# Performance work log

Measured on AMD Instinct MI355X. Metric: run time of the kernel, lower is better.

Reference implementation:

```python
import jax, jax.numpy as jnp
import numpy as np

HEAD_NUM = 16
KEY_DIM = 64
EMBED = 1024
KV_OUT = HEAD_NUM * KEY_DIM  # 1024


def setup_inputs() -> dict:
    key = jax.random.key(0)
    ks = jax.random.split(key, 11)
    B, L, E = 2, 2048, EMBED
    scale = 0.02
    return {
        "query": jax.random.normal(ks[0], (B, L, E), jnp.float32),
        "key": jax.random.normal(ks[1], (B, L, E), jnp.float32),
        "value": jax.random.normal(ks[2], (B, L, E), jnp.float32),
        "W_Query": jax.random.normal(ks[3], (E, KV_OUT), jnp.float32) * scale,
        "W_Key": jax.random.normal(ks[4], (E, KV_OUT), jnp.float32) * scale,
        "W_Value": jax.random.normal(ks[5], (E, KV_OUT), jnp.float32) * scale,
        "W_Output": jax.random.normal(ks[6], (KV_OUT, E), jnp.float32) * scale,
        "B_Query": jnp.zeros((KV_OUT,), jnp.float32),
        "B_Key": jnp.zeros((KV_OUT,), jnp.float32),
        "B_Value": jnp.zeros((KV_OUT,), jnp.float32),
        "B_Output": jnp.zeros((E,), jnp.float32),
    }


def reference(query, key, value, W_Query, W_Key, W_Value, W_Output,
              B_Query, B_Key, B_Value, B_Output):
    B, Lq, E = query.shape
    Lk = key.shape[1]
    H, D = HEAD_NUM, KEY_DIM
    # QKV projections + bias
    q = query @ W_Query + B_Query            # [B, Lq, H*D]
    k = key @ W_Key + B_Key                  # [B, Lk, H*D]
    v = value @ W_Value + B_Value            # [B, Lk, H*D]
    # tf.split(axis=2) per head == reshape to [B, L, H, D]
    q = q.reshape(B, Lq, H, D)
    k = k.reshape(B, Lk, H, D)
    v = v.reshape(B, Lk, H, D)
    # scaled dot-product attention (no mask, dropout=0)
    scores = jnp.einsum("bqhd,bkhd->bhqk", q, k) / (D ** 0.5)
    probs = jax.nn.softmax(scores, axis=-1)
    out = jnp.einsum("bhqk,bkhd->bqhd", probs, v)  # [B, Lq, H, D]
    out = out.reshape(B, Lq, H * D)
    return out @ W_Output + B_Output
```

## Files before the change

kernel.cpp:

```cpp
#include <hip/hip_runtime.h>

using u16 = unsigned short;
using u32 = unsigned int;

typedef __attribute__((ext_vector_type(8))) short bf16x8;
typedef __attribute__((ext_vector_type(4))) float f32x4;
typedef __attribute__((ext_vector_type(4))) u32 u32x4;
typedef __attribute__((ext_vector_type(2))) u32 u32x2;
typedef __attribute__((ext_vector_type(4))) _Float16 f16x4;
typedef __attribute__((ext_vector_type(8))) _Float16 f16x8;

#define MFMA_BF16_K32(a, b, c) __builtin_amdgcn_mfma_f32_16x16x32_bf16((a), (b), (c), 0, 0, 0)
#define MFMA_F16_K32(a, b, c) __builtin_amdgcn_mfma_f32_16x16x32_f16((a), (b), (c), 0, 0, 0)

#define QSCALE 0.18033688011112042f

extern "C" __device__ float __ocml_native_exp2_f32(float);

__device__ __forceinline__ u16 f2bf(float f) {
  u32 u = __builtin_bit_cast(u32, f);
  return (u16)((u + 0x7fffu + ((u >> 16) & 1u)) >> 16);
}

__device__ __forceinline__ u32 pk_f16(float a, float b) {
  auto v = __builtin_amdgcn_cvt_pkrtz(a, b);
  return __builtin_bit_cast(u32, v);
}

__device__ __forceinline__ void load_lds16(const void* g, void* l) {
  __builtin_amdgcn_global_load_lds((__attribute__((address_space(1))) void*)g,
                                   (__attribute__((address_space(3))) void*)l,
                                   16, 0, 0);
}

#define W0 asm volatile("s_waitcnt vmcnt(0)" ::: "memory")
#define W3 asm volatile("s_waitcnt vmcnt(3)" ::: "memory")
#define W4 asm volatile("s_waitcnt vmcnt(4)" ::: "memory")
#define W8 asm volatile("s_waitcnt vmcnt(8)" ::: "memory")
#define LGKM0 asm volatile("s_waitcnt lgkmcnt(0)" ::: "memory")
#define BARRIER                      \
  do {                               \
    __builtin_amdgcn_s_barrier();    \
    asm volatile("" ::: "memory");   \
  } while (0)

__global__ __launch_bounds__(256) void cvt_all_kernel(
    const float* __restrict__ q, const float* __restrict__ k, const float* __restrict__ v,
    u16* __restrict__ oq, u16* __restrict__ ok, u16* __restrict__ ov,
    const float* __restrict__ w0, const float* __restrict__ w1,
    const float* __restrict__ w2, const float* __restrict__ w3,
    u16* __restrict__ d0, u16* __restrict__ d1,
    u16* __restrict__ d2, u16* __restrict__ d3) {
  const int id = blockIdx.x;
  const int tid = threadIdx.x;
  if (id < 6144) {
    const int z = id >> 11, bx = id & 2047;
    const float* s = z == 0 ? q : z == 1 ? k : v;
    u16* d = z == 0 ? oq : z == 1 ? ok : ov;
    int i = (bx * 256 + tid) * 8;
    f32x4 a = *(const f32x4*)(s + i);
    f32x4 b = *(const f32x4*)(s + i + 4);
    u32x4 o;
    o.x = (u32)f2bf(a.x) | ((u32)f2bf(a.y) << 16);
    o.y = (u32)f2bf(a.z) | ((u32)f2bf(a.w) << 16);
    o.z = (u32)f2bf(b.x) | ((u32)f2bf(b.y) << 16);
    o.w = (u32)f2bf(b.z) | ((u32)f2bf(b.w) << 16);
    *(u32x4*)(d + i) = o;
    return;
  }
  __shared__ float t[64][65];
  const int r0 = id - 6144;
  const int z = r0 >> 8, rr0 = r0 & 255;
  const int bx = rr0 & 15, by = rr0 >> 4;
  const float* src = z == 0 ? w0 : z == 1 ? w1 : z == 2 ? w2 : w3;
  u16* dst = z == 0 ? d0 : z == 1 ? d1 : z == 2 ? d2 : d3;
  const float scale = (z == 0) ? QSCALE : 1.0f;
  const int r = tid >> 4, c4 = (tid & 15) * 4;
#pragma unroll
  for (int i = 0; i < 4; ++i) {
    int row = r + i * 16;
    f32x4 vv = *(const f32x4*)(src + (by * 64 + row) * 1024 + bx * 64 + c4);
    t[row][c4 + 0] = vv.x;
    t[row][c4 + 1] = vv.y;
    t[row][c4 + 2] = vv.z;
    t[row][c4 + 3] = vv.w;
  }
  __syncthreads();
  const int rw = tid >> 2, cc = (tid & 3) * 16;
  alignas(16) u16 tmp[16];
#pragma unroll
  for (int j = 0; j < 16; ++j) tmp[j] = f2bf(t[cc + j][rw] * scale);
  u32x4* outp = (u32x4*)(dst + (bx * 64 + rw) * 1024 + by * 64 + cc);
  outp[0] = *(const u32x4*)&tmp[0];
  outp[1] = *(const u32x4*)&tmp[8];
}

#define QKV_STAGE(BUF, KB)                                                    \
  {                                                                           \
    _Pragma("unroll") for (int t = 0; t < 2; ++t) {                           \
      int c = (wave * 2 + t) * 64 + lane;                                     \
      int row = c >> 2, pc = c & 3, sc = pc ^ ((row >> 1) & 3);               \
      load_lds16(A + (m0 + row) * 1024 + (KB) * 32 + sc * 8,                  \
                 &As[BUF][((wave * 2 + t) * 64) * 8]);                        \
    }                                                                         \
    _Pragma("unroll") for (int t = 0; t < 2; ++t) {                           \
      int c = (wave * 2 + t) * 64 + lane;                                     \
      int row = c >> 2, pc = c & 3, sc = pc ^ ((row >> 1) & 3);               \
      load_lds16(Bt + (n0 + row) * 1024 + (KB) * 32 + sc * 8,                 \
                 &Bs[BUF][((wave * 2 + t) * 64) * 8]);                        \
    }                                                                         \
  }

__global__ __launch_bounds__(256) void gemm_qkv_kernel(
    const u16* __restrict__ x0, const u16* __restrict__ x1, const u16* __restrict__ x2,
    const u16* __restrict__ w0, const u16* __restrict__ w1, const u16* __restrict__ w2,
    const float* __restrict__ b0, const float* __restrict__ b1, const float* __restrict__ b2,
    u16* __restrict__ c0, u16* __restrict__ c1, u16* __restrict__ vt) {
  __shared__ u16 As[2][128 * 32];
  __shared__ u16 Bs[2][128 * 32];
  const int lid = blockIdx.x;
  const int xcd = lid & 7, rr = lid >> 3;
  const int nb = rr & 7, slot = rr >> 3;
  const int g = slot * 8 + xcd;
  const int z = g >> 5, m_idx = g & 31;
  const u16* A = z == 0 ? x0 : z == 1 ? x1 : x2;
  const u16* Bt = z == 0 ? w0 : z == 1 ? w1 : w2;
  const float* bias = z == 0 ? b0 : z == 1 ? b1 : b2;
  const float bscale = z == 0 ? QSCALE : 1.0f;
  const int tid = threadIdx.x;
  const int wave = tid >> 6, lane = tid & 63;
  const int l16 = lane & 15, quad = lane >> 4;
  const int wm = wave >> 1, wn = wave & 1;
  const int m0 = m_idx * 128, n0 = nb * 128;

  f32x4 acc[4][4];
  const f32x4 zf = {0.f, 0.f, 0.f, 0.f};
#pragma unroll
  for (int i = 0; i < 4; ++i)
#pragma unroll
    for (int j = 0; j < 4; ++j) acc[i][j] = zf;

  QKV_STAGE(0, 0);
  QKV_STAGE(1, 1);

  const int chq = (l16 >> 1) & 3;
  for (int kb = 0; kb < 32; ++kb) {
    const int cur = kb & 1;
    if (kb < 31) W4; else W0;
    BARRIER;
    bf16x8 af[4], bfv[4];
#pragma unroll
    for (int mt = 0; mt < 4; ++mt)
      af[mt] = *(const bf16x8*)&As[cur][(wm * 64 + mt * 16 + l16) * 32 + (quad ^ chq) * 8];
#pragma unroll
    for (int nt = 0; nt < 4; ++nt)
      bfv[nt] = *(const bf16x8*)&Bs[cur][(wn * 64 + nt * 16 + l16) * 32 + (quad ^ chq) * 8];
#pragma unroll
    for (int mt = 0; mt < 4; ++mt)
#pragma unroll
      for (int nt = 0; nt < 4; ++nt) acc[mt][nt] = MFMA_BF16_K32(af[mt], bfv[nt], acc[mt][nt]);
    LGKM0;
    BARRIER;
    if (kb + 2 < 32) QKV_STAGE(cur, kb + 2);
  }

  float bv[4];
#pragma unroll
  for (int nt = 0; nt < 4; ++nt) bv[nt] = bias[n0 + wn * 64 + nt * 16 + l16] * bscale;
  if (z != 2) {
    u16* C = z == 0 ? c0 : c1;
#pragma unroll
    for (int mt = 0; mt < 4; ++mt)
#pragma unroll
      for (int nt = 0; nt < 4; ++nt)
#pragma unroll
        for (int r = 0; r < 4; ++r) {
          int row = m0 + wm * 64 + mt * 16 + quad * 4 + r;
          int col = n0 + wn * 64 + nt * 16 + l16;
          C[row * 1024 + col] = f2bf(acc[mt][nt][r] + bv[nt]);
        }
  } else {
#pragma unroll
    for (int p = 0; p < 2; ++p) {
#pragma unroll
      for (int nt = 0; nt < 4; ++nt) {
        const int mte = p * 2, mto = p * 2 + 1;
        f16x4 he, ho;
#pragma unroll
        for (int r = 0; r < 4; ++r) {
          he[r] = (_Float16)(acc[mte][nt][r] + bv[nt]);
          ho[r] = (_Float16)(acc[mto][nt][r] + bv[nt]);
        }
        u32x2 hou = __builtin_bit_cast(u32x2, ho);
        u32x2 hox;
        hox.x = (u32)__shfl_xor((int)hou.x, 32);
        hox.y = (u32)__shfl_xor((int)hou.y, 32);
        int kvb = m0 + wm * 64 + mte * 16 + quad * 4;
        int bb = kvb >> 11, kv = kvb & 2047;
        int kb2 = kv >> 7, w = (kv >> 5) & 3;
        int col = n0 + wn * 64 + nt * 16 + l16;
        int h = col >> 6, dt = (col >> 4) & 3, ld = col & 15;
        int pair = bb * 16 + h;
        u32x2 heu = __builtin_bit_cast(u32x2, he);
        u32x4 outv;
        outv.x = heu.x;
        outv.y = heu.y;
        outv.z = hox.x;
        outv.w = hox.y;
        u16* dst = vt + ((((pair * 16 + kb2) * 4 + w) * 4 + dt) * 512) + (quad * 16 + ld) * 8;
        *(u32x4*)dst = outv;
      }
    }
  }
}

#define OUT_STAGE(BUF, KB)                                                    \
  {                                                                           \
    {                                                                         \
      int c = wave * 64 + lane;                                               \
      int row = c >> 2, pc = c & 3, sc = pc ^ ((row >> 1) & 3);               \
      load_lds16(A + (m0 + row) * 1024 + (KB) * 32 + sc * 8,                  \
                 &As[BUF][(wave * 64) * 8]);                                  \
    }                                                                         \
    _Pragma("unroll") for (int t = 0; t < 2; ++t) {                           \
      int c = (wave * 2 + t) * 64 + lane;                                     \
      int row = c >> 2, pc = c & 3, sc = pc ^ ((row >> 1) & 3);               \
      load_lds16(Bt + (n0 + row) * 1024 + (KB) * 32 + sc * 8,                 \
                 &Bs[BUF][((wave * 2 + t) * 64) * 8]);                        \
    }                                                                         \
  }

__global__ __launch_bounds__(256) void gemm_out_kernel(const u16* __restrict__ A,
                                                       const u16* __restrict__ Bt,
                                                       const float* __restrict__ bias,
                                                       float* __restrict__ C) {
  __shared__ u16 As[2][64 * 32];
  __shared__ u16 Bs[2][128 * 32];
  const int lid = blockIdx.x;
  const int xcd = lid & 7, rr = lid >> 3;
  const int nb = rr & 7, slot = rr >> 3;
  const int by = slot * 8 + xcd;
  const int tid = threadIdx.x;
  const int wave = tid >> 6, lane = tid & 63;
  const int l16 = lane & 15, quad = lane >> 4;
  const int m0 = by * 64, n0 = nb * 128;

  f32x4 acc[4][2];
  const f32x4 zf = {0.f, 0.f, 0.f, 0.f};
#pragma unroll
  for (int i = 0; i < 4; ++i)
#pragma unroll
    for (int j = 0; j < 2; ++j) acc[i][j] = zf;

  OUT_STAGE(0, 0);
  OUT_STAGE(1, 1);

  const int chq = (l16 >> 1) & 3;
  for (int kb = 0; kb < 32; ++kb) {
    const int cur = kb & 1;
    if (kb < 31) W3; else W0;
    BARRIER;
    bf16x8 af[4], bfv[2];
#pragma unroll
    for (int mt = 0; mt < 4; ++mt)
      af[mt] = *(const bf16x8*)&As[cur][(mt * 16 + l16) * 32 + (quad ^ chq) * 8];
#pragma unroll
    for (int nt = 0; nt < 2; ++nt)
      bfv[nt] = *(const bf16x8*)&Bs[cur][(wave * 32 + nt * 16 + l16) * 32 + (quad ^ chq) * 8];
#pragma unroll
    for (int mt = 0; mt < 4; ++mt)
#pragma unroll
      for (int nt = 0; nt < 2; ++nt) acc[mt][nt] = MFMA_BF16_K32(af[mt], bfv[nt], acc[mt][nt]);
    LGKM0;
    BARRIER;
    if (kb + 2 < 32) OUT_STAGE(cur, kb + 2);
  }

  float bv[2];
#pragma unroll
  for (int nt = 0; nt < 2; ++nt) bv[nt] = bias[n0 + wave * 32 + nt * 16 + l16];
#pragma unroll
  for (int mt = 0; mt < 4; ++mt)
#pragma unroll
    for (int nt = 0; nt < 2; ++nt)
#pragma unroll
      for (int r = 0; r < 4; ++r) {
        int row = m0 + mt * 16 + quad * 4 + r;
        int col = n0 + wave * 32 + nt * 16 + l16;
        C[row * 1024 + col] = acc[mt][nt][r] + bv[nt];
      }
}

#define QK_EXP(CUR)                                                               \
  _Pragma("unroll") for (int c2 = 0; c2 < 2; ++c2) {                              \
    const int chunk = wave * 2 + c2;                                              \
    f32x4 s_acc[4];                                                               \
    _Pragma("unroll") for (int qn = 0; qn < 4; ++qn) s_acc[qn] = zf;              \
    _Pragma("unroll") for (int ks = 0; ks < 2; ++ks) {                            \
      bf16x8 kf = *(const bf16x8*)&k_lds[CUR][(chunk * 16 + l16) * 64 +           \
                                              ((ks * 4 + quad) ^ l7) * 8];        \
      _Pragma("unroll") for (int qn = 0; qn < 4; ++qn)                            \
        s_acc[qn] = MFMA_BF16_K32(kf, qf[qn][ks], s_acc[qn]);                     \
    }                                                                             \
    _Pragma("unroll") for (int qn = 0; qn < 4; ++qn) {                            \
      float e0 = __ocml_native_exp2_f32(s_acc[qn].x);                             \
      float e1 = __ocml_native_exp2_f32(s_acc[qn].y);                             \
      float e2 = __ocml_native_exp2_f32(s_acc[qn].z);                             \
      float e3 = __ocml_native_exp2_f32(s_acc[qn].w);                             \
      lp[qn] += (e0 + e1) + (e2 + e3);                                            \
      if (c2 == 0) {                                                              \
        p01[qn] = pk_f16(e0, e1);                                                 \
        p23[qn] = pk_f16(e2, e3);                                                 \
      } else {                                                                    \
        s01[qn] = pk_f16(e0, e1);                                                 \
        s23[qn] = pk_f16(e2, e3);                                                 \
      }                                                                           \
    }                                                                             \
  }

#define FLASH_BODY(KB, CUR, VCUR, VNXT, PFV, PFK, WAIT)                           \
  {                                                                               \
    BARRIER;                                                                      \
    if (PFV) {                                                                    \
      const u16* vp = Vh + ((KB) + 1) * 8192;                                     \
      _Pragma("unroll") for (int dt = 0; dt < 4; ++dt)                            \
        VNXT[dt] = *(const f16x8*)(vp + (wave * 4 + dt) * 512 + lane * 8);        \
    }                                                                             \
    u32 p01[4], p23[4], s01[4], s23[4];                                           \
    QK_EXP(CUR)                                                                   \
    f16x8 paf[4];                                                                 \
    _Pragma("unroll") for (int qn = 0; qn < 4; ++qn) {                            \
      u32x4 tv;                                                                   \
      tv.x = p01[qn];                                                             \
      tv.y = p23[qn];                                                             \
      tv.z = (u32)__shfl_xor((int)s01[qn], 32);                                   \
      tv.w = (u32)__shfl_xor((int)s23[qn], 32);                                   \
      paf[qn] = __builtin_bit_cast(f16x8, tv);                                    \
    }                                                                             \
    LGKM0;                                                                        \
    BARRIER;                                                                      \
    if (PFK) {                                                                    \
      const int kv0 = ((KB) + 2) * 128;                                           \
      _Pragma("unroll") for (int t = 0; t < 4; ++t) {                             \
        int c = (t * 4 + wave) * 64 + lane;                                       \
        int row = c >> 3, sc8 = (c & 7) ^ (row & 7);                              \
        load_lds16(Kh + (kv0 + row) * 1024 + sc8 * 8,                             \
                   &k_lds[CUR][((t * 4 + wave) * 64) * 8]);                       \
      }                                                                           \
    }                                                                             \
    WAIT;                                                                         \
    _Pragma("unroll") for (int dt = 0; dt < 4; ++dt)                              \
      _Pragma("unroll") for (int qn = 0; qn < 4; ++qn)                            \
        o_acc[qn][dt] = MFMA_F16_K32(paf[qn], VCUR[dt], o_acc[qn][dt]);           \
  }

__global__ __launch_bounds__(256, 2) void flash_kernel(const u16* __restrict__ Q,
                                                       const u16* __restrict__ K,
                                                       const u16* __restrict__ Vt,
                                                       u16* __restrict__ O) {
  __shared__ u16 k_lds[2][128 * 64];
  __shared__ float lred[4][64];
  __shared__ float lfin[64];
  const int tid = threadIdx.x;
  const int wave = tid >> 6, lane = tid & 63;
  const int l16 = lane & 15, quad = lane >> 4;
  const int l7 = l16 & 7;
  const int id = blockIdx.x;
  const int xcd = id & 7, slot = id >> 3;
  const int pair = xcd * 4 + (slot & 3);
  const int qb = slot >> 2;
  const int b = pair >> 4, h = pair & 15;
  const u16* Qh = Q + (b * 2048 + qb * 64) * 1024 + h * 64;
  const u16* Kh = K + b * 2048 * 1024 + h * 64;
  const u16* Vh = Vt + pair * 131072;

#pragma unroll
  for (int t = 0; t < 2; ++t) {
    int c = (t * 4 + wave) * 64 + lane;
    int row = c >> 3, sc8 = (c & 7) ^ (row & 7);
    load_lds16(Qh + row * 1024 + sc8 * 8, &k_lds[0][((t * 4 + wave) * 64) * 8]);
  }
  W0;
  __syncthreads();
  bf16x8 qf[4][2];
#pragma unroll
  for (int qn = 0; qn < 4; ++qn)
#pragma unroll
    for (int ks = 0; ks < 2; ++ks)
      qf[qn][ks] = *(const bf16x8*)&k_lds[0][(qn * 16 + l16) * 64 + (((ks * 4 + quad) ^ l7)) * 8];
  __syncthreads();

#pragma unroll
  for (int t = 0; t < 4; ++t) {
    int c = (t * 4 + wave) * 64 + lane;
    int row = c >> 3, sc8 = (c & 7) ^ (row & 7);
    load_lds16(Kh + row * 1024 + sc8 * 8, &k_lds[0][((t * 4 + wave) * 64) * 8]);
  }
  f16x8 vregA[4], vregB[4];
#pragma unroll
  for (int dt = 0; dt < 4; ++dt)
    vregA[dt] = *(const f16x8*)(Vh + (wave * 4 + dt) * 512 + lane * 8);
#pragma unroll
  for (int t = 0; t < 4; ++t) {
    int c = (t * 4 + wave) * 64 + lane;
    int row = c >> 3, sc8 = (c & 7) ^ (row & 7);
    load_lds16(Kh + (128 + row) * 1024 + sc8 * 8, &k_lds[1][((t * 4 + wave) * 64) * 8]);
  }
  W8;

  f32x4 o_acc[4][4];
  const f32x4 zf = {0.f, 0.f, 0.f, 0.f};
#pragma unroll
  for (int qn = 0; qn < 4; ++qn)
#pragma unroll
    for (int dt = 0; dt < 4; ++dt) o_acc[qn][dt] = zf;
  float lp[4] = {0.f, 0.f, 0.f, 0.f};

  for (int kb2 = 0; kb2 < 7; ++kb2) {
    const int kb = kb2 * 2;
    FLASH_BODY(kb, 0, vregA, vregB, true, true, W8);
    FLASH_BODY(kb + 1, 1, vregB, vregA, true, true, W8);
  }
  FLASH_BODY(14, 0, vregA, vregB, true, false, W4);
  FLASH_BODY(15, 1, vregB, vregA, false, false, W0);

#pragma unroll
  for (int qn = 0; qn < 4; ++qn) {
    lp[qn] += __shfl_xor(lp[qn], 16);
    lp[qn] += __shfl_xor(lp[qn], 32);
  }
  if (quad == 0) {
#pragma unroll
    for (int qn = 0; qn < 4; ++qn) lred[wave][qn * 16 + l16] = lp[qn];
  }
  float* bufA = (float*)&k_lds[0][0];
  float* bufB = (float*)&k_lds[1][0];
  if (wave == 1 || wave == 3) {
    float* buf = (wave == 1) ? bufA : bufB;
#pragma unroll
    for (int qm = 0; qm < 4; ++qm)
#pragma unroll
      for (int dt = 0; dt < 4; ++dt)
        *(f32x4*)&buf[(((qm * 4 + dt) * 4 + quad) * 16 + l16) * 4] = o_acc[qm][dt];
  }
  __syncthreads();
  if (tid < 64) lfin[tid] = lred[0][tid] + lred[1][tid] + lred[2][tid] + lred[3][tid];
  if (wave == 0 || wave == 2) {
    float* buf = (wave == 0) ? bufA : bufB;
#pragma unroll
    for (int qm = 0; qm < 4; ++qm)
#pragma unroll
      for (int dt = 0; dt < 4; ++dt)
        o_acc[qm][dt] += *(const f32x4*)&buf[(((qm * 4 + dt) * 4 + quad) * 16 + l16) * 4];
  }
  __syncthreads();
  if (wave == 2) {
#pragma unroll
    for (int qm = 0; qm < 4; ++qm)
#pragma unroll
      for (int dt = 0; dt < 4; ++dt)
        *(f32x4*)&bufA[(((qm * 4 + dt) * 4 + quad) * 16 + l16) * 4] = o_acc[qm][dt];
  }
  __syncthreads();
  if (wave == 0) {
#pragma unroll
    for (int qm = 0; qm < 4; ++qm)
#pragma unroll
      for (int dt = 0; dt < 4; ++dt)
        o_acc[qm][dt] += *(const f32x4*)&bufA[(((qm * 4 + dt) * 4 + quad) * 16 + l16) * 4];
#pragma unroll
    for (int qm = 0; qm < 4; ++qm)
#pragma unroll
      for (int r = 0; r < 4; ++r) {
        int qrow = qm * 16 + quad * 4 + r;
        float inv = 1.0f / lfin[qrow];
        int row = b * 2048 + qb * 64 + qrow;
#pragma unroll
        for (int dt = 0; dt < 4; ++dt)
          O[row * 1024 + h * 64 + dt * 16 + l16] = f2bf(o_acc[qm][dt][r] * inv);
      }
  }
}

extern "C" void kernel_launch(void* const* d_in, const int* in_sizes, int n_in,
                              void* d_out, int out_size, void* d_ws, size_t ws_size,
                              hipStream_t stream) {
  const float* q = (const float*)d_in[0];
  const float* k = (const float*)d_in[1];
  const float* v = (const float*)d_in[2];
  const float* Wq = (const float*)d_in[3];
  const float* Wk = (const float*)d_in[4];
  const float* Wv = (const float*)d_in[5];
  const float* Wo = (const float*)d_in[6];
  const float* Bq = (const float*)d_in[7];
  const float* Bk = (const float*)d_in[8];
  const float* Bv = (const float*)d_in[9];
  const float* Bo = (const float*)d_in[10];
  float* out = (float*)d_out;

  char* w = (char*)d_ws;
  const size_t MB = 1u << 20;
  u16* xq = (u16*)(w + 0 * MB);
  u16* xk = (u16*)(w + 8 * MB);
  u16* xv = (u16*)(w + 16 * MB);
  u16* wqt = (u16*)(w + 24 * MB);
  u16* wkt = (u16*)(w + 26 * MB);
  u16* wvt = (u16*)(w + 28 * MB);
  u16* wot = (u16*)(w + 30 * MB);
  u16* Qp = (u16*)(w + 32 * MB);
  u16* Kp = (u16*)(w + 40 * MB);
  u16* Vtr = (u16*)(w + 48 * MB);
  u16* At = (u16*)(w + 56 * MB);

  cvt_all_kernel<<<dim3(7168), 256, 0, stream>>>(q, k, v, xq, xk, xv,
                                                 Wq, Wk, Wv, Wo, wqt, wkt, wvt, wot);
  gemm_qkv_kernel<<<dim3(768), 256, 0, stream>>>(xq, xk, xv, wqt, wkt, wvt,
                                                 Bq, Bk, Bv, Qp, Kp, Vtr);
  flash_kernel<<<dim3(1024), 256, 0, stream>>>(Qp, Kp, Vtr, At);
  gemm_out_kernel<<<dim3(512), 256, 0, stream>>>(At, wot, Bo, out);
}
```

Measured before the change: 218.4 us.

## Fuse fp32-to-bf16 activation conversion into QKV GEMM A-tile loading

Removes the separate conversion pass over the query, key and value activations. The QKV GEMM now loads fp32 A tiles into registers, converts them to bf16 and writes them to LDS itself, using a register double-buffered pipeline with hand-tuned vmcnt waits. This drops a full read and write of the three activation tensors, which is 72 MB of traffic. In exchange each GEMM block re-reads fp32 A once per N-block, which doubles A bytes per tile. It also adds register pressure and VALU conversion work inside the main loop.

```diff
diff --git a/kernel.cpp b/kernel.cpp
--- a/kernel.cpp
+++ b/kernel.cpp
@@ -34,8 +34,10 @@
 }
 
 #define W0 asm volatile("s_waitcnt vmcnt(0)" ::: "memory")
+#define W2 asm volatile("s_waitcnt vmcnt(2)" ::: "memory")
 #define W3 asm volatile("s_waitcnt vmcnt(3)" ::: "memory")
 #define W4 asm volatile("s_waitcnt vmcnt(4)" ::: "memory")
+#define W6 asm volatile("s_waitcnt vmcnt(6)" ::: "memory")
 #define W8 asm volatile("s_waitcnt vmcnt(8)" ::: "memory")
 #define LGKM0 asm volatile("s_waitcnt lgkmcnt(0)" ::: "memory")
 #define BARRIER                      \
@@ -44,32 +46,14 @@
     asm volatile("" ::: "memory");   \
   } while (0)
 
-__global__ __launch_bounds__(256) void cvt_all_kernel(
-    const float* __restrict__ q, const float* __restrict__ k, const float* __restrict__ v,
-    u16* __restrict__ oq, u16* __restrict__ ok, u16* __restrict__ ov,
+__global__ __launch_bounds__(256) void cvt_w_kernel(
     const float* __restrict__ w0, const float* __restrict__ w1,
     const float* __restrict__ w2, const float* __restrict__ w3,
     u16* __restrict__ d0, u16* __restrict__ d1,
     u16* __restrict__ d2, u16* __restrict__ d3) {
-  const int id = blockIdx.x;
   const int tid = threadIdx.x;
-  if (id < 6144) {
-    const int z = id >> 11, bx = id & 2047;
-    const float* s = z == 0 ? q : z == 1 ? k : v;
-    u16* d = z == 0 ? oq : z == 1 ? ok : ov;
-    int i = (bx * 256 + tid) * 8;
-    f32x4 a = *(const f32x4*)(s + i);
-    f32x4 b = *(const f32x4*)(s + i + 4);
-    u32x4 o;
-    o.x = (u32)f2bf(a.x) | ((u32)f2bf(a.y) << 16);
-    o.y = (u32)f2bf(a.z) | ((u32)f2bf(a.w) << 16);
-    o.z = (u32)f2bf(b.x) | ((u32)f2bf(b.y) << 16);
-    o.w = (u32)f2bf(b.z) | ((u32)f2bf(b.w) << 16);
-    *(u32x4*)(d + i) = o;
-    return;
-  }
   __shared__ float t[64][65];
-  const int r0 = id - 6144;
+  const int r0 = blockIdx.x;
   const int z = r0 >> 8, rr0 = r0 & 255;
   const int bx = rr0 & 15, by = rr0 >> 4;
   const float* src = z == 0 ? w0 : z == 1 ? w1 : z == 2 ? w2 : w3;
@@ -95,24 +79,65 @@
   outp[1] = *(const u32x4*)&tmp[8];
 }
 
-#define QKV_STAGE(BUF, KB)                                                    \
+#define QKV_ISSUE_A(AREG, KB)                                                 \
+  _Pragma("unroll") for (int t = 0; t < 2; ++t) {                             \
+    int c = (wave * 2 + t) * 64 + lane;                                       \
+    int row = c >> 2, pc = c & 3, sc = pc ^ ((row >> 1) & 3);                 \
+    const float* asrc = Af + (m0 + row) * 1024 + (KB) * 32 + sc * 8;          \
+    AREG[t][0] = *(const f32x4*)asrc;                                         \
+    AREG[t][1] = *(const f32x4*)(asrc + 4);                                   \
+  }
+
+#define QKV_ISSUE_B(BUF, KB)                                                  \
+  _Pragma("unroll") for (int t = 0; t < 2; ++t) {                             \
+    int c = (wave * 2 + t) * 64 + lane;                                       \
+    int row = c >> 2, pc = c & 3, sc = pc ^ ((row >> 1) & 3);                 \
+    load_lds16(Bt + (n0 + row) * 1024 + (KB) * 32 + sc * 8,                   \
+               &Bs[BUF][((wave * 2 + t) * 64) * 8]);                          \
+  }
+
+#define QKV_COMMIT_A(AREG, BUF)                                               \
+  _Pragma("unroll") for (int t = 0; t < 2; ++t) {                             \
+    int c = (wave * 2 + t) * 64 + lane;                                       \
+    u32x4 o;                                                                  \
+    o.x = (u32)f2bf(AREG[t][0].x) | ((u32)f2bf(AREG[t][0].y) << 16);          \
+    o.y = (u32)f2bf(AREG[t][0].z) | ((u32)f2bf(AREG[t][0].w) << 16);          \
+    o.z = (u32)f2bf(AREG[t][1].x) | ((u32)f2bf(AREG[t][1].y) << 16);          \
+    o.w = (u32)f2bf(AREG[t][1].z) | ((u32)f2bf(AREG[t][1].w) << 16);          \
+    *(u32x4*)&As[BUF][c * 8] = o;                                             \
+  }
+
+#define QKV_ITER(KB, CUR, AI, AC, DO_ISSUE, DO_COMMIT, TOPW, CMW, NOT_LAST)   \
   {                                                                           \
-    _Pragma("unroll") for (int t = 0; t < 2; ++t) {                           \
-      int c = (wave * 2 + t) * 64 + lane;                                     \
-      int row = c >> 2, pc = c & 3, sc = pc ^ ((row >> 1) & 3);               \
-      load_lds16(A + (m0 + row) * 1024 + (KB) * 32 + sc * 8,                  \
-                 &As[BUF][((wave * 2 + t) * 64) * 8]);                        \
+    TOPW;                                                                     \
+    LGKM0;                                                                    \
+    BARRIER;                                                                  \
+    bf16x8 af[4], bfv[4];                                                     \
+    _Pragma("unroll") for (int mt = 0; mt < 4; ++mt)                          \
+      af[mt] = *(const bf16x8*)&As[CUR][(wm * 64 + mt * 16 + l16) * 32 +      \
+                                        (quad ^ chq) * 8];                    \
+    _Pragma("unroll") for (int nt = 0; nt < 4; ++nt)                          \
+      bfv[nt] = *(const bf16x8*)&Bs[CUR][(wn * 64 + nt * 16 + l16) * 32 +     \
+                                         (quad ^ chq) * 8];                   \
+    _Pragma("unroll") for (int mt = 0; mt < 4; ++mt)                          \
+      _Pragma("unroll") for (int nt = 0; nt < 4; ++nt)                        \
+        acc[mt][nt] = MFMA_BF16_K32(af[mt], bfv[nt], acc[mt][nt]);            \
+    if (NOT_LAST) {                                                           \
+      LGKM0;                                                                  \
+      BARRIER;                                                                \
     }                                                                         \
-    _Pragma("unroll") for (int t = 0; t < 2; ++t) {                           \
-      int c = (wave * 2 + t) * 64 + lane;                                     \
-      int row = c >> 2, pc = c & 3, sc = pc ^ ((row >> 1) & 3);               \
-      load_lds16(Bt + (n0 + row) * 1024 + (KB) * 32 + sc * 8,                 \
-                 &Bs[BUF][((wave * 2 + t) * 64) * 8]);                        \
+    if (DO_ISSUE) {                                                           \
+      QKV_ISSUE_A(AI, (KB) + 2);                                              \
+      QKV_ISSUE_B(CUR, (KB) + 2);                                             \
     }                                                                         \
+    if (DO_COMMIT) {                                                          \
+      CMW;                                                                    \
+      QKV_COMMIT_A(AC, (CUR) ^ 1);                                            \
+    }                                                                         \
   }
 
 __global__ __launch_bounds__(256) void gemm_qkv_kernel(
-    const u16* __restrict__ x0, const u16* __restrict__ x1, const u16* __restrict__ x2,
+    const float* __restrict__ x0, const float* __restrict__ x1, const float* __restrict__ x2,
     const u16* __restrict__ w0, const u16* __restrict__ w1, const u16* __restrict__ w2,
     const float* __restrict__ b0, const float* __restrict__ b1, const float* __restrict__ b2,
     u16* __restrict__ c0, u16* __restrict__ c1, u16* __restrict__ vt) {
@@ -123,7 +148,7 @@
   const int nb = rr & 7, slot = rr >> 3;
   const int g = slot * 8 + xcd;
   const int z = g >> 5, m_idx = g & 31;
-  const u16* A = z == 0 ? x0 : z == 1 ? x1 : x2;
+  const float* Af = z == 0 ? x0 : z == 1 ? x1 : x2;
   const u16* Bt = z == 0 ? w0 : z == 1 ? w1 : w2;
   const float* bias = z == 0 ? b0 : z == 1 ? b1 : b2;
   const float bscale = z == 0 ? QSCALE : 1.0f;
@@ -140,29 +165,24 @@
 #pragma unroll
     for (int j = 0; j < 4; ++j) acc[i][j] = zf;
 
-  QKV_STAGE(0, 0);
-  QKV_STAGE(1, 1);
+  f32x4 aregA[2][2], aregB[2][2];
+  QKV_ISSUE_A(aregA, 0);
+  QKV_ISSUE_B(0, 0);
+  QKV_ISSUE_A(aregB, 1);
+  QKV_ISSUE_B(1, 1);
+  W8;
+  QKV_COMMIT_A(aregA, 0);
 
   const int chq = (l16 >> 1) & 3;
-  for (int kb = 0; kb < 32; ++kb) {
-    const int cur = kb & 1;
-    if (kb < 31) W4; else W0;
-    BARRIER;
-    bf16x8 af[4], bfv[4];
-#pragma unroll
-    for (int mt = 0; mt < 4; ++mt)
-      af[mt] = *(const bf16x8*)&As[cur][(wm * 64 + mt * 16 + l16) * 32 + (quad ^ chq) * 8];
-#pragma unroll
-    for (int nt = 0; nt < 4; ++nt)
-      bfv[nt] = *(const bf16x8*)&Bs[cur][(wn * 64 + nt * 16 + l16) * 32 + (quad ^ chq) * 8];
-#pragma unroll
-    for (int mt = 0; mt < 4; ++mt)
-#pragma unroll
-      for (int nt = 0; nt < 4; ++nt) acc[mt][nt] = MFMA_BF16_K32(af[mt], bfv[nt], acc[mt][nt]);
-    LGKM0;
-    BARRIER;
-    if (kb + 2 < 32) QKV_STAGE(cur, kb + 2);
-  }
+  for (int kb2 = 0; kb2 < 14; ++kb2) {
+    const int kb = kb2 * 2;
+    QKV_ITER(kb, 0, aregA, aregB, true, true, W6, W8, true);
+    QKV_ITER(kb + 1, 1, aregB, aregA, true, true, W6, W8, true);
+  }
+  QKV_ITER(28, 0, aregA, aregB, true, true, W6, W8, true);
+  QKV_ITER(29, 1, aregB, aregA, true, true, W6, W8, true);
+  QKV_ITER(30, 0, aregA, aregB, false, true, W6, W2, true);
+  QKV_ITER(31, 1, aregB, aregA, false, false, W0, W0, false);
 
   float bv[4];
 #pragma unroll
@@ -500,9 +520,6 @@
 
   char* w = (char*)d_ws;
   const size_t MB = 1u << 20;
-  u16* xq = (u16*)(w + 0 * MB);
-  u16* xk = (u16*)(w + 8 * MB);
-  u16* xv = (u16*)(w + 16 * MB);
   u16* wqt = (u16*)(w + 24 * MB);
   u16* wkt = (u16*)(w + 26 * MB);
   u16* wvt = (u16*)(w + 28 * MB);
@@ -512,9 +529,8 @@
   u16* Vtr = (u16*)(w + 48 * MB);
   u16* At = (u16*)(w + 56 * MB);
 
-  cvt_all_kernel<<<dim3(7168), 256, 0, stream>>>(q, k, v, xq, xk, xv,
-                                                 Wq, Wk, Wv, Wo, wqt, wkt, wvt, wot);
-  gemm_qkv_kernel<<<dim3(768), 256, 0, stream>>>(xq, xk, xv, wqt, wkt, wvt,
+  cvt_w_kernel<<<dim3(1024), 256, 0, stream>>>(Wq, Wk, Wv, Wo, wqt, wkt, wvt, wot);
+  gemm_qkv_kernel<<<dim3(768), 256, 0, stream>>>(q, k, v, wqt, wkt, wvt,
                                                  Bq, Bk, Bv, Qp, Kp, Vtr);
   flash_kernel<<<dim3(1024), 256, 0, stream>>>(Qp, Kp, Vtr, At);
   gemm_out_kernel<<<dim3(512), 256, 0, stream>>>(At, wot, Bo, out);
```

Measured after the change: 243.0 us. 1.11x slower.

## Triple-buffer K tiles in LDS to drop one barrier per flash iteration

Applied to the files above, without the earlier changes.

The flash kernel's K staging goes from two LDS buffers to three, rotating through them with a 6-step unrolled loop. The prefetch for block kb+2 now writes a buffer nobody is reading, so the mid-iteration LGKM wait and barrier are removed and a vmcnt wait moves to the top of each step. The aim is to cut barrier stalls and let K prefetch overlap the QK and PV math. In exchange LDS use per block grows by 16 KB, which could reduce occupancy, and the hand-tuned vmcnt counts must match the number of loads still in flight.

```diff
diff --git a/kernel.cpp b/kernel.cpp
--- a/kernel.cpp
+++ b/kernel.cpp
@@ -37,6 +37,7 @@
 #define W3 asm volatile("s_waitcnt vmcnt(3)" ::: "memory")
 #define W4 asm volatile("s_waitcnt vmcnt(4)" ::: "memory")
 #define W8 asm volatile("s_waitcnt vmcnt(8)" ::: "memory")
+#define W12 asm volatile("s_waitcnt vmcnt(12)" ::: "memory")
 #define LGKM0 asm volatile("s_waitcnt lgkmcnt(0)" ::: "memory")
 #define BARRIER                      \
   do {                               \
@@ -318,8 +319,9 @@
     }                                                                             \
   }
 
-#define FLASH_BODY(KB, CUR, VCUR, VNXT, PFV, PFK, WAIT)                           \
+#define FB(KB, KBUF, NBUF, VCUR, VNXT, PFV, PFK, TOPW, PVW)                       \
   {                                                                               \
+    TOPW;                                                                         \
     BARRIER;                                                                      \
     if (PFV) {                                                                    \
       const u16* vp = Vh + ((KB) + 1) * 8192;                                     \
@@ -327,7 +329,7 @@
         VNXT[dt] = *(const f16x8*)(vp + (wave * 4 + dt) * 512 + lane * 8);        \
     }                                                                             \
     u32 p01[4], p23[4], s01[4], s23[4];                                           \
-    QK_EXP(CUR)                                                                   \
+    QK_EXP(KBUF)                                                                  \
     f16x8 paf[4];                                                                 \
     _Pragma("unroll") for (int qn = 0; qn < 4; ++qn) {                            \
       u32x4 tv;                                                                   \
@@ -337,18 +339,16 @@
       tv.w = (u32)__shfl_xor((int)s23[qn], 32);                                   \
       paf[qn] = __builtin_bit_cast(f16x8, tv);                                    \
     }                                                                             \
-    LGKM0;                                                                        \
-    BARRIER;                                                                      \
     if (PFK) {                                                                    \
       const int kv0 = ((KB) + 2) * 128;                                           \
       _Pragma("unroll") for (int t = 0; t < 4; ++t) {                             \
         int c = (t * 4 + wave) * 64 + lane;                                       \
         int row = c >> 3, sc8 = (c & 7) ^ (row & 7);                              \
         load_lds16(Kh + (kv0 + row) * 1024 + sc8 * 8,                             \
-                   &k_lds[CUR][((t * 4 + wave) * 64) * 8]);                       \
+                   &k_lds[NBUF][((t * 4 + wave) * 64) * 8]);                      \
       }                                                                           \
     }                                                                             \
-    WAIT;                                                                         \
+    PVW;                                                                          \
     _Pragma("unroll") for (int dt = 0; dt < 4; ++dt)                              \
       _Pragma("unroll") for (int qn = 0; qn < 4; ++qn)                            \
         o_acc[qn][dt] = MFMA_F16_K32(paf[qn], VCUR[dt], o_acc[qn][dt]);           \
@@ -358,7 +358,7 @@
                                                        const u16* __restrict__ K,
                                                        const u16* __restrict__ Vt,
                                                        u16* __restrict__ O) {
-  __shared__ u16 k_lds[2][128 * 64];
+  __shared__ u16 k_lds[3][128 * 64];
   __shared__ float lred[4][64];
   __shared__ float lfin[64];
   const int tid = threadIdx.x;
@@ -406,7 +406,6 @@
     int row = c >> 3, sc8 = (c & 7) ^ (row & 7);
     load_lds16(Kh + (128 + row) * 1024 + sc8 * 8, &k_lds[1][((t * 4 + wave) * 64) * 8]);
   }
-  W8;
 
   f32x4 o_acc[4][4];
   const f32x4 zf = {0.f, 0.f, 0.f, 0.f};
@@ -416,13 +415,19 @@
     for (int dt = 0; dt < 4; ++dt) o_acc[qn][dt] = zf;
   float lp[4] = {0.f, 0.f, 0.f, 0.f};
 
-  for (int kb2 = 0; kb2 < 7; ++kb2) {
-    const int kb = kb2 * 2;
-    FLASH_BODY(kb, 0, vregA, vregB, true, true, W8);
-    FLASH_BODY(kb + 1, 1, vregB, vregA, true, true, W8);
-  }
-  FLASH_BODY(14, 0, vregA, vregB, true, false, W4);
-  FLASH_BODY(15, 1, vregB, vregA, false, false, W0);
+  for (int kb6 = 0; kb6 < 2; ++kb6) {
+    const int kb = kb6 * 6;
+    FB(kb + 0, 0, 2, vregA, vregB, true, true, W8, W12);
+    FB(kb + 1, 1, 0, vregB, vregA, true, true, W8, W12);
+    FB(kb + 2, 2, 1, vregA, vregB, true, true, W8, W12);
+    FB(kb + 3, 0, 2, vregB, vregA, true, true, W8, W12);
+    FB(kb + 4, 1, 0, vregA, vregB, true, true, W8, W12);
+    FB(kb + 5, 2, 1, vregB, vregA, true, true, W8, W12);
+  }
+  FB(12, 0, 2, vregA, vregB, true, true, W8, W12);
+  FB(13, 1, 0, vregB, vregA, true, true, W8, W12);
+  FB(14, 2, 1, vregA, vregB, true, false, W8, W8);
+  FB(15, 0, 2, vregB, vregA, false, false, W4, W0);
 
 #pragma unroll
   for (int qn = 0; qn < 4; ++qn) {
```

New measurement: 298.8 us. +36.8%, slower.

## Fuse fp32-to-bf16 activation conversion into QKV GEMM tile loads

Applied to the files above, without the earlier changes.

Drops the separate pass that converts query/key/value activations to bf16. The QKV GEMM now streams fp32 activations straight into LDS with an 8-chunk XOR swizzle and converts them to bf16 in registers via v_cvt_pk_bf16_f32 before the MFMAs. This removes one full read and write of the 48MB of activations, plus a large conversion launch. In exchange the A-tile LDS footprint and global load traffic per stage double, and each k-step does extra conversion ALU work.

```diff
diff --git a/kernel.cpp b/kernel.cpp
--- a/kernel.cpp
+++ b/kernel.cpp
@@ -22,6 +22,12 @@
   return (u16)((u + 0x7fffu + ((u >> 16) & 1u)) >> 16);
 }
 
+__device__ __forceinline__ u32 pk_bf16(float a, float b) {
+  u32 r;
+  asm("v_cvt_pk_bf16_f32 %0, %1, %2" : "=v"(r) : "v"(a), "v"(b));
+  return r;
+}
+
 __device__ __forceinline__ u32 pk_f16(float a, float b) {
   auto v = __builtin_amdgcn_cvt_pkrtz(a, b);
   return __builtin_bit_cast(u32, v);
@@ -36,6 +42,7 @@
 #define W0 asm volatile("s_waitcnt vmcnt(0)" ::: "memory")
 #define W3 asm volatile("s_waitcnt vmcnt(3)" ::: "memory")
 #define W4 asm volatile("s_waitcnt vmcnt(4)" ::: "memory")
+#define W6 asm volatile("s_waitcnt vmcnt(6)" ::: "memory")
 #define W8 asm volatile("s_waitcnt vmcnt(8)" ::: "memory")
 #define LGKM0 asm volatile("s_waitcnt lgkmcnt(0)" ::: "memory")
 #define BARRIER                      \
@@ -44,32 +51,14 @@
     asm volatile("" ::: "memory");   \
   } while (0)
 
-__global__ __launch_bounds__(256) void cvt_all_kernel(
-    const float* __restrict__ q, const float* __restrict__ k, const float* __restrict__ v,
-    u16* __restrict__ oq, u16* __restrict__ ok, u16* __restrict__ ov,
+__global__ __launch_bounds__(256) void cvt_w_kernel(
     const float* __restrict__ w0, const float* __restrict__ w1,
     const float* __restrict__ w2, const float* __restrict__ w3,
     u16* __restrict__ d0, u16* __restrict__ d1,
     u16* __restrict__ d2, u16* __restrict__ d3) {
-  const int id = blockIdx.x;
   const int tid = threadIdx.x;
-  if (id < 6144) {
-    const int z = id >> 11, bx = id & 2047;
-    const float* s = z == 0 ? q : z == 1 ? k : v;
-    u16* d = z == 0 ? oq : z == 1 ? ok : ov;
-    int i = (bx * 256 + tid) * 8;
-    f32x4 a = *(const f32x4*)(s + i);
-    f32x4 b = *(const f32x4*)(s + i + 4);
-    u32x4 o;
-    o.x = (u32)f2bf(a.x) | ((u32)f2bf(a.y) << 16);
-    o.y = (u32)f2bf(a.z) | ((u32)f2bf(a.w) << 16);
-    o.z = (u32)f2bf(b.x) | ((u32)f2bf(b.y) << 16);
-    o.w = (u32)f2bf(b.z) | ((u32)f2bf(b.w) << 16);
-    *(u32x4*)(d + i) = o;
-    return;
-  }
   __shared__ float t[64][65];
-  const int r0 = id - 6144;
+  const int r0 = blockIdx.x;
   const int z = r0 >> 8, rr0 = r0 & 255;
   const int bx = rr0 & 15, by = rr0 >> 4;
   const float* src = z == 0 ? w0 : z == 1 ? w1 : z == 2 ? w2 : w3;
@@ -97,11 +86,11 @@
 
 #define QKV_STAGE(BUF, KB)                                                    \
   {                                                                           \
-    _Pragma("unroll") for (int t = 0; t < 2; ++t) {                           \
-      int c = (wave * 2 + t) * 64 + lane;                                     \
-      int row = c >> 2, pc = c & 3, sc = pc ^ ((row >> 1) & 3);               \
-      load_lds16(A + (m0 + row) * 1024 + (KB) * 32 + sc * 8,                  \
-                 &As[BUF][((wave * 2 + t) * 64) * 8]);                        \
+    _Pragma("unroll") for (int t = 0; t < 4; ++t) {                           \
+      int c = (wave * 4 + t) * 64 + lane;                                     \
+      int row = c >> 3, sc8 = (c & 7) ^ (row & 7);                            \
+      load_lds16(Af + (m0 + row) * 1024 + (KB) * 32 + sc8 * 4,                \
+                 &Asf[BUF][((wave * 4 + t) * 64) * 4]);                       \
     }                                                                         \
     _Pragma("unroll") for (int t = 0; t < 2; ++t) {                           \
       int c = (wave * 2 + t) * 64 + lane;                                     \
@@ -112,24 +101,25 @@
   }
 
 __global__ __launch_bounds__(256) void gemm_qkv_kernel(
-    const u16* __restrict__ x0, const u16* __restrict__ x1, const u16* __restrict__ x2,
+    const float* __restrict__ x0, const float* __restrict__ x1, const float* __restrict__ x2,
     const u16* __restrict__ w0, const u16* __restrict__ w1, const u16* __restrict__ w2,
     const float* __restrict__ b0, const float* __restrict__ b1, const float* __restrict__ b2,
     u16* __restrict__ c0, u16* __restrict__ c1, u16* __restrict__ vt) {
-  __shared__ u16 As[2][128 * 32];
+  __shared__ float Asf[2][128 * 32];
   __shared__ u16 Bs[2][128 * 32];
   const int lid = blockIdx.x;
   const int xcd = lid & 7, rr = lid >> 3;
   const int nb = rr & 7, slot = rr >> 3;
   const int g = slot * 8 + xcd;
   const int z = g >> 5, m_idx = g & 31;
-  const u16* A = z == 0 ? x0 : z == 1 ? x1 : x2;
+  const float* Af = z == 0 ? x0 : z == 1 ? x1 : x2;
   const u16* Bt = z == 0 ? w0 : z == 1 ? w1 : w2;
   const float* bias = z == 0 ? b0 : z == 1 ? b1 : b2;
   const float bscale = z == 0 ? QSCALE : 1.0f;
   const int tid = threadIdx.x;
   const int wave = tid >> 6, lane = tid & 63;
   const int l16 = lane & 15, quad = lane >> 4;
+  const int l7 = l16 & 7;
   const int wm = wave >> 1, wn = wave & 1;
   const int m0 = m_idx * 128, n0 = nb * 128;
 
@@ -144,14 +134,25 @@
   QKV_STAGE(1, 1);
 
   const int chq = (l16 >> 1) & 3;
+  const int p1 = (2 * quad) ^ l7;
+  const int p2 = (2 * quad + 1) ^ l7;
   for (int kb = 0; kb < 32; ++kb) {
     const int cur = kb & 1;
-    if (kb < 31) W4; else W0;
+    if (kb < 31) W6; else W0;
     BARRIER;
     bf16x8 af[4], bfv[4];
 #pragma unroll
-    for (int mt = 0; mt < 4; ++mt)
-      af[mt] = *(const bf16x8*)&As[cur][(wm * 64 + mt * 16 + l16) * 32 + (quad ^ chq) * 8];
+    for (int mt = 0; mt < 4; ++mt) {
+      int arow = wm * 64 + mt * 16 + l16;
+      f32x4 a0 = *(const f32x4*)&Asf[cur][arow * 32 + p1 * 4];
+      f32x4 a1 = *(const f32x4*)&Asf[cur][arow * 32 + p2 * 4];
+      u32x4 pw;
+      pw.x = pk_bf16(a0.x, a0.y);
+      pw.y = pk_bf16(a0.z, a0.w);
+      pw.z = pk_bf16(a1.x, a1.y);
+      pw.w = pk_bf16(a1.z, a1.w);
+      af[mt] = __builtin_bit_cast(bf16x8, pw);
+    }
 #pragma unroll
     for (int nt = 0; nt < 4; ++nt)
       bfv[nt] = *(const bf16x8*)&Bs[cur][(wn * 64 + nt * 16 + l16) * 32 + (quad ^ chq) * 8];
@@ -500,9 +501,6 @@
 
   char* w = (char*)d_ws;
   const size_t MB = 1u << 20;
-  u16* xq = (u16*)(w + 0 * MB);
-  u16* xk = (u16*)(w + 8 * MB);
-  u16* xv = (u16*)(w + 16 * MB);
   u16* wqt = (u16*)(w + 24 * MB);
   u16* wkt = (u16*)(w + 26 * MB);
   u16* wvt = (u16*)(w + 28 * MB);
@@ -512,9 +510,8 @@
   u16* Vtr = (u16*)(w + 48 * MB);
   u16* At = (u16*)(w + 56 * MB);
 
-  cvt_all_kernel<<<dim3(7168), 256, 0, stream>>>(q, k, v, xq, xk, xv,
-                                                 Wq, Wk, Wv, Wo, wqt, wkt, wvt, wot);
-  gemm_qkv_kernel<<<dim3(768), 256, 0, stream>>>(xq, xk, xv, wqt, wkt, wvt,
+  cvt_w_kernel<<<dim3(1024), 256, 0, stream>>>(Wq, Wk, Wv, Wo, wqt, wkt, wvt, wot);
+  gemm_qkv_kernel<<<dim3(768), 256, 0, stream>>>(q, k, v, wqt, wkt, wvt,
                                                  Bq, Bk, Bv, Qp, Kp, Vtr);
   flash_kernel<<<dim3(1024), 256, 0, stream>>>(Qp, Kp, Vtr, At);
   gemm_out_kernel<<<dim3(512), 256, 0, stream>>>(At, wot, Bo, out);
```

Measured after the change: 225.8 us. 1.03x slower.
